# Kernel tuning notes

Measured on AMD Instinct MI355X. Metric: run time of the kernel, lower is better.

Reference implementation:

```python
import jax, jax.numpy as jnp
import numpy as np

B, N, D, H = 2, 2048, 384, 8
Dh = D // H          # 48
G = Dh // 3          # 16 3-vectors per head
EPS = 1e-5


def setup_inputs() -> dict:
    key = jax.random.key(0)
    ks = jax.random.split(key, 8)
    x = jax.random.normal(ks[0], (B, N, D), dtype=jnp.float32)
    # per-node SE(3) frames: proper rotation matrices via QR of random Gaussians
    raw = jax.random.normal(ks[1], (B, N, 3, 3), dtype=jnp.float32)
    q, r = jnp.linalg.qr(raw)
    sign = jnp.sign(jnp.diagonal(r, axis1=-2, axis2=-1))
    frames = q * sign[..., None, :]
    s = 1.0 / np.sqrt(D)
    Wq = jax.random.normal(ks[2], (D, D), dtype=jnp.float32) * s
    Wk = jax.random.normal(ks[3], (D, D), dtype=jnp.float32) * s
    Wv = jax.random.normal(ks[4], (D, D), dtype=jnp.float32) * s
    Wo = jax.random.normal(ks[5], (D, D), dtype=jnp.float32) * s
    bo = jnp.zeros((D,), dtype=jnp.float32)
    gamma = jnp.ones((D,), dtype=jnp.float32)
    beta = jnp.zeros((D,), dtype=jnp.float32)
    return {"x": x, "frames": frames, "Wq": Wq, "Wk": Wk, "Wv": Wv,
            "Wo": Wo, "bo": bo, "gamma": gamma, "beta": beta}


def _rotate(frames, t):
    # t: [B,N,H,Dh] -> rotate each 3-vector chunk by the node's frame R_i
    b, n, h, dh = t.shape
    t3 = t.reshape(b, n, h, dh // 3, 3)
    r3 = jnp.einsum('bnij,bnhgj->bnhgi', frames, t3)
    return r3.reshape(b, n, h, dh)


def reference(x, frames, Wq, Wk, Wv, Wo, bo, gamma, beta):
    b, n, d = x.shape
    Q = (x @ Wq.T).reshape(b, n, H, Dh)
    K = (x @ Wk.T).reshape(b, n, H, Dh)
    V = (x @ Wv.T).reshape(b, n, H, Dh)
    # SE(3) frame-conditioned attention: rotate Q,K into each node's local frame
    Qr = _rotate(frames, Q)
    Kr = _rotate(frames, K)
    scores = jnp.einsum('bqhd,bkhd->bhqk', Qr, Kr) / np.sqrt(Dh)
    attn = jax.nn.softmax(scores, axis=-1)
    out = jnp.einsum('bhqk,bkhd->bqhd', attn, V).reshape(b, n, d)
    out = out @ Wo.T + bo          # out_proj; dropout is identity in eval
    y = x + out                     # residual
    mu = jnp.mean(y, axis=-1, keepdims=True)
    var = jnp.var(y, axis=-1, keepdims=True)
    return (y - mu) * jax.lax.rsqrt(var + EPS) * gamma + beta
```

## Files before the change

kernel.cpp:

```cpp
#include <hip/hip_runtime.h>
#include <hip/hip_bf16.h>
#include <math.h>

constexpr int B = 2, N = 2048, D = 384, H = 8, Dh = 48;
constexpr int M = B * N;
constexpr float EPS = 1e-5f;
constexpr int WSZ = 384 * 384;

typedef short bf16x8 __attribute__((ext_vector_type(8)));
typedef float f32x4 __attribute__((ext_vector_type(4)));

#if __has_builtin(__builtin_amdgcn_exp2f)
#define EXP2(x) __builtin_amdgcn_exp2f(x)
#else
#define EXP2(x) exp2f(x)
#endif

__device__ __forceinline__ ushort f2bf(float f) {
  union { float f; uint u; } v; v.f = f;
  uint r = v.u + 0x7fffu + ((v.u >> 16) & 1u);
  return (ushort)(r >> 16);
}
__device__ __forceinline__ float bf2f(ushort u) {
  union { uint u; float f; } v; v.u = ((uint)u) << 16;
  return v.f;
}
__device__ __forceinline__ uint pk_bf16(float lo, float hi) {
  union { __hip_bfloat162 h; uint u; } v;
  v.h = __float22bfloat162_rn(make_float2(lo, hi));
  return v.u;
}

__device__ __forceinline__ void gload16(const void* g, void* lds) {
  __builtin_amdgcn_global_load_lds(
      (const __attribute__((address_space(1))) unsigned int*)g,
      (__attribute__((address_space(3))) unsigned int*)lds, 16, 0, 0);
}

__global__ __launch_bounds__(256) void pack_all(
    const float* __restrict__ x, const float* __restrict__ Wq,
    const float* __restrict__ Wk, const float* __restrict__ Wv,
    const float* __restrict__ Wo, ushort* __restrict__ xbf,
    ushort* __restrict__ Wqkv, ushort* __restrict__ Wobf) {
  constexpr int XSZ = M * 384;
  int i = (blockIdx.x * 256 + threadIdx.x) * 8;
  const float* src; ushort* dst; int off;
  if (i < XSZ) { src = x; dst = xbf; off = i; }
  else {
    int j = i - XSZ;
    if (j < WSZ)          { src = Wq; dst = Wqkv;           off = j; }
    else if (j < 2 * WSZ) { src = Wk; dst = Wqkv + WSZ;     off = j - WSZ; }
    else if (j < 3 * WSZ) { src = Wv; dst = Wqkv + 2 * WSZ; off = j - 2 * WSZ; }
    else                  { src = Wo; dst = Wobf;           off = j - 3 * WSZ; }
  }
  float4 a = *(const float4*)(src + off);
  float4 b = *(const float4*)(src + off + 4);
  uint4 o;
  o.x = pk_bf16(a.x, a.y);
  o.y = pk_bf16(a.z, a.w);
  o.z = pk_bf16(b.x, b.y);
  o.w = pk_bf16(b.z, b.w);
  *(uint4*)(dst + off) = o;
}

__global__ __launch_bounds__(256) void gemm_qkv(
    const ushort* __restrict__ Abf, const ushort* __restrict__ Wbf,
    const float* __restrict__ F, ushort* __restrict__ Qpad,
    ushort* __restrict__ Kpad, ushort* __restrict__ Vt, float qscale) {
  __shared__ __align__(16) ushort SH[128 * 96];
  ushort* Asm = SH;
  ushort* Bsm = SH + 4096;
  const int tid = threadIdx.x, w = tid >> 6, lane = tid & 63;
  const int lq = lane & 15, g = lane >> 4;
  const int brow = blockIdx.y * 128;
  const int bx = blockIdx.x;
  const int bcol = bx * 96;
  const int wr0 = (w >> 1) * 64, wc0 = (w & 1) * 48;
  const int srow = lane >> 2, scol = (lane & 3) * 8;

  f32x4 acc[4][3];
#pragma unroll
  for (int mi = 0; mi < 4; ++mi)
#pragma unroll
    for (int ni = 0; ni < 3; ++ni) acc[mi][ni] = f32x4{0.f, 0.f, 0.f, 0.f};

  for (int kt = 0; kt < 384; kt += 32) {
    __syncthreads();
    for (int s = w; s < 14; s += 4) {
      if (s < 8)
        gload16(Abf + (size_t)(brow + s * 16 + srow) * 384 + kt + scol, Asm + s * 512);
      else
        gload16(Wbf + (size_t)(bcol + (s - 8) * 16 + srow) * 384 + kt + scol,
                Bsm + (s - 8) * 512);
    }
    __syncthreads();
    bf16x8 a[4], b[3];
#pragma unroll
    for (int mi = 0; mi < 4; ++mi)
      a[mi] = *(const bf16x8*)(Asm + (wr0 + mi * 16 + lq) * 32 + g * 8);
#pragma unroll
    for (int ni = 0; ni < 3; ++ni)
      b[ni] = *(const bf16x8*)(Bsm + (wc0 + ni * 16 + lq) * 32 + g * 8);
#pragma unroll
    for (int mi = 0; mi < 4; ++mi)
#pragma unroll
      for (int ni = 0; ni < 3; ++ni)
        acc[mi][ni] = __builtin_amdgcn_mfma_f32_16x16x32_bf16(a[mi], b[ni], acc[mi][ni], 0, 0, 0);
  }

  if (bx >= 8) {
#pragma unroll
    for (int mi = 0; mi < 4; ++mi)
#pragma unroll
      for (int ni = 0; ni < 3; ++ni) {
        int vcol = (bx - 8) * 96 + wc0 + ni * 16 + lq;
        int hh = vcol / 48, dh = vcol - hh * 48;
#pragma unroll
        for (int r = 0; r < 4; ++r) {
          int row = brow + wr0 + mi * 16 + g * 4 + r;
          int bb = row >> 11, nn = row & 2047;
          Vt[((size_t)(bb * H + hh) * 48 + dh) * N + nn] = f2bf(acc[mi][ni][r]);
        }
      }
    return;
  }

  __syncthreads();
#pragma unroll
  for (int mi = 0; mi < 4; ++mi)
#pragma unroll
    for (int ni = 0; ni < 3; ++ni) {
      int col = wc0 + ni * 16 + lq;
#pragma unroll
      for (int r = 0; r < 4; ++r)
        SH[(wr0 + mi * 16 + g * 4 + r) * 96 + col] = f2bf(acc[mi][ni][r]);
    }
  __syncthreads();

  ushort* dstm = (bx < 4) ? Qpad : Kpad;
  const int hb = (bx & 3) * 2;
  const float scale = (bx < 4) ? qscale : 1.0f;
#pragma unroll
  for (int it = 0; it < 2; ++it) {
    int task = tid + it * 256;
    int row = task >> 2;
    int hh = (task >> 1) & 1;
    int half = task & 1;
    int bn = brow + row;
    const float* R = F + (size_t)bn * 9;
    float r0 = R[0], r1 = R[1], r2 = R[2];
    float r3 = R[3], r4 = R[4], r5 = R[5];
    float r6 = R[6], r7 = R[7], r8 = R[8];
    const ushort* src = SH + row * 96 + hh * 48 + half * 24;
    uint u[12];
    *(uint4*)(u)     = *(const uint4*)(src);
    *(uint4*)(u + 4) = *(const uint4*)(src + 8);
    *(uint4*)(u + 8) = *(const uint4*)(src + 16);
    float f[24];
#pragma unroll
    for (int j = 0; j < 12; ++j) {
      f[2 * j] = bf2f((ushort)u[j]);
      f[2 * j + 1] = bf2f((ushort)(u[j] >> 16));
    }
    float o[24];
#pragma unroll
    for (int t = 0; t < 8; ++t) {
      float v0 = f[3 * t], v1 = f[3 * t + 1], v2 = f[3 * t + 2];
      o[3 * t]     = (r0 * v0 + r1 * v1 + r2 * v2) * scale;
      o[3 * t + 1] = (r3 * v0 + r4 * v1 + r5 * v2) * scale;
      o[3 * t + 2] = (r6 * v0 + r7 * v1 + r8 * v2) * scale;
    }
    uint ow[12];
#pragma unroll
    for (int j = 0; j < 12; ++j) ow[j] = pk_bf16(o[2 * j], o[2 * j + 1]);
    ushort* dp = dstm + (size_t)bn * 512 + (hb + hh) * 64 + half * 24;
    *(uint4*)(dp)      = *(uint4*)(ow);
    *(uint4*)(dp + 8)  = *(uint4*)(ow + 4);
    *(uint4*)(dp + 16) = *(uint4*)(ow + 8);
    if (half) {
      uint4 z = make_uint4(0, 0, 0, 0);
      ushort* zp = dstm + (size_t)bn * 512 + (hb + hh) * 64 + 48;
      *(uint4*)(zp) = z;
      *(uint4*)(zp + 8) = z;
    }
  }
}

__global__ __launch_bounds__(128) void attn_mfma(
    const ushort* __restrict__ Qpad, const ushort* __restrict__ Kpad,
    const ushort* __restrict__ Vt, ushort* __restrict__ Pacc,
    float* __restrict__ Pml) {
  __shared__ __align__(16) ushort SH[8192];
  ushort* K0 = SH;
  ushort* K1 = SH + 4096;

  const int bid = blockIdx.x;
  const int wg = (bid & 7) * 128 + (bid >> 3);
  const int qt = wg & 31;
  const int rest = wg >> 5;
  const int h = rest & 7;
  const int b = (rest >> 3) & 1;
  const int half = rest >> 4;
  const int kt0 = half * 1024;
  const int tid = threadIdx.x;
  const int w = tid >> 6;
  const int lane = tid & 63;
  const int lq = lane & 15;
  const int g = lane >> 4;
  const int l7 = lq & 7;
  const int srow8 = lane >> 3;
  const int c8 = (lane & 7) ^ srow8;

  bf16x8 qf[2][2];
  {
    const ushort* qb = Qpad + ((size_t)(b * N) + qt * 64 + w * 32) * 512 + h * 64;
#pragma unroll
    for (int i = 0; i < 2; ++i)
#pragma unroll
      for (int kd = 0; kd < 2; ++kd)
        qf[i][kd] = *(const bf16x8*)(qb + (size_t)(i * 16 + lq) * 512 + kd * 32 + g * 8);
  }

  const ushort* kg[4];
#pragma unroll
  for (int j = 0; j < 4; ++j) {
    int s = w + 2 * j;
    int ki = (s >> 2) * 32 + (s & 1) * 16 + (srow8 >> 2) * 8 + ((s >> 1) & 1) * 4 + (srow8 & 3);
    kg[j] = Kpad + ((size_t)(b * N) + kt0 + ki) * 512 + h * 64 + c8 * 8;
  }
  const ushort* vbase = Vt + ((size_t)(b * H + h) * 48 + lq) * (size_t)N + kt0 + g * 8;

  auto stage = [&](ushort* kb) {
#pragma unroll
    for (int j = 0; j < 4; ++j) {
      gload16(kg[j], kb + (w + 2 * j) * 512);
      kg[j] += 64 * 512;
    }
  };

  float m[2] = {-3.0e38f, -3.0e38f}, l[2] = {0.f, 0.f};
  f32x4 oacc[2][3];
#pragma unroll
  for (int i = 0; i < 2; ++i)
#pragma unroll
    for (int d = 0; d < 3; ++d) oacc[i][d] = f32x4{0.f, 0.f, 0.f, 0.f};

  stage(K0);
  __syncthreads();
  int cur = 0;

  for (int t = 0; t < 16; ++t) {
    if (t < 15) stage(cur ? K0 : K1);
    const ushort* Kc = cur ? K1 : K0;

    bf16x8 vf[2][3];
#pragma unroll
    for (int ks = 0; ks < 2; ++ks)
#pragma unroll
      for (int d = 0; d < 3; ++d)
        vf[ks][d] = *(const bf16x8*)(vbase + (size_t)(d * 16) * N + ks * 32);

    f32x4 st[2][4];
#pragma unroll
    for (int i = 0; i < 2; ++i)
#pragma unroll
      for (int t4 = 0; t4 < 4; ++t4) st[i][t4] = f32x4{0.f, 0.f, 0.f, 0.f};
#pragma unroll
    for (int t4 = 0; t4 < 4; ++t4) {
      bf16x8 a0 = *(const bf16x8*)(Kc + (t4 * 16 + lq) * 64 + ((g ^ l7) * 8));
      bf16x8 a1 = *(const bf16x8*)(Kc + (t4 * 16 + lq) * 64 + (((g + 4) ^ l7) * 8));
#pragma unroll
      for (int i = 0; i < 2; ++i) {
        st[i][t4] = __builtin_amdgcn_mfma_f32_16x16x32_bf16(a0, qf[i][0], st[i][t4], 0, 0, 0);
        st[i][t4] = __builtin_amdgcn_mfma_f32_16x16x32_bf16(a1, qf[i][1], st[i][t4], 0, 0, 0);
      }
    }

    float tmax[2];
#pragma unroll
    for (int i = 0; i < 2; ++i) {
      float t0 = st[i][0][0];
#pragma unroll
      for (int t4 = 0; t4 < 4; ++t4)
#pragma unroll
        for (int r = 0; r < 4; ++r) t0 = fmaxf(t0, st[i][t4][r]);
      t0 = fmaxf(t0, __shfl_xor(t0, 16));
      t0 = fmaxf(t0, __shfl_xor(t0, 32));
      tmax[i] = t0;
    }
    bool need = (tmax[0] > m[0] + 8.0f) | (tmax[1] > m[1] + 8.0f);
    if (__ballot(need)) {
#pragma unroll
      for (int i = 0; i < 2; ++i) {
        float mnew = fmaxf(m[i], tmax[i]);
        float corr = EXP2(m[i] - mnew);
        m[i] = mnew;
        l[i] *= corr;
#pragma unroll
        for (int r = 0; r < 4; ++r) {
          float cr = __shfl(corr, g * 4 + r);
#pragma unroll
          for (int d = 0; d < 3; ++d) oacc[i][d][r] *= cr;
        }
      }
    }

    bf16x8 pf[2][2];
#pragma unroll
    for (int i = 0; i < 2; ++i) {
      float ps = 0.f;
      uint u0[4], u1[4];
#pragma unroll
      for (int t4 = 0; t4 < 4; ++t4) {
        float p0 = EXP2(st[i][t4][0] - m[i]);
        float p1 = EXP2(st[i][t4][1] - m[i]);
        float p2 = EXP2(st[i][t4][2] - m[i]);
        float p3 = EXP2(st[i][t4][3] - m[i]);
        ps += (p0 + p1) + (p2 + p3);
        if (t4 < 2) {
          u0[(t4 & 1) * 2]     = pk_bf16(p0, p1);
          u0[(t4 & 1) * 2 + 1] = pk_bf16(p2, p3);
        } else {
          u1[(t4 & 1) * 2]     = pk_bf16(p0, p1);
          u1[(t4 & 1) * 2 + 1] = pk_bf16(p2, p3);
        }
      }
      ps += __shfl_xor(ps, 16);
      ps += __shfl_xor(ps, 32);
      l[i] += ps;
      union { uint4 q; bf16x8 v; } c0, c1;
      c0.q = make_uint4(u0[0], u0[1], u0[2], u0[3]);
      c1.q = make_uint4(u1[0], u1[1], u1[2], u1[3]);
      pf[i][0] = c0.v;
      pf[i][1] = c1.v;
    }

#pragma unroll
    for (int ks = 0; ks < 2; ++ks)
#pragma unroll
      for (int i = 0; i < 2; ++i)
#pragma unroll
        for (int d = 0; d < 3; ++d)
          oacc[i][d] = __builtin_amdgcn_mfma_f32_16x16x32_bf16(pf[i][ks], vf[ks][d], oacc[i][d], 0, 0, 0);

    vbase += 64;
    __syncthreads();
    cur ^= 1;
  }

#pragma unroll
  for (int i = 0; i < 2; ++i) {
    const size_t pr0 = ((size_t)((half * B + b) * H + h)) * N + qt * 64 + (w * 2 + i) * 16;
#pragma unroll
    for (int d = 0; d < 3; ++d)
#pragma unroll
      for (int r = 0; r < 4; ++r)
        Pacc[(pr0 + g * 4 + r) * 48 + d * 16 + lq] = f2bf(oacc[i][d][r]);
    if (g == 0) {
      Pml[(pr0 + lq) * 2] = m[i];
      Pml[(pr0 + lq) * 2 + 1] = l[i];
    }
  }
}

__global__ __launch_bounds__(256) void gemm_out_ln(
    const ushort* __restrict__ Pacc, const float* __restrict__ Pml,
    const ushort* __restrict__ Wbf, const float* __restrict__ x,
    const float* __restrict__ bo, const float* __restrict__ gamma,
    const float* __restrict__ beta, float* __restrict__ out) {
  __shared__ ushort Asm[16 * 32];
  __shared__ ushort Bsm[384 * 32];
  __shared__ float red[4][16][2];
  __shared__ float Wm[16][8][2];
  const int tid = threadIdx.x, w = tid >> 6, lane = tid & 63;
  const int lq = lane & 15, g = lane >> 4;
  const int brow = blockIdx.x * 16;
  const int srow = lane >> 2, scol = (lane & 3) * 8;

  if (tid < 128) {
    int r = tid >> 3, hh = tid & 7;
    int gr = brow + r;
    int bb = gr >> 11, nn = gr & 2047;
    size_t i0 = ((size_t)(bb * H + hh)) * N + nn;
    size_t i1 = ((size_t)((B + bb) * H + hh)) * N + nn;
    float m0 = Pml[i0 * 2], l0 = Pml[i0 * 2 + 1];
    float m1 = Pml[i1 * 2], l1 = Pml[i1 * 2 + 1];
    float mm = fmaxf(m0, m1);
    float e0 = EXP2(m0 - mm), e1 = EXP2(m1 - mm);
    float inv = 1.f / (l0 * e0 + l1 * e1);
    Wm[r][hh][0] = e0 * inv;
    Wm[r][hh][1] = e1 * inv;
  }
  __syncthreads();

  f32x4 acc[6];
#pragma unroll
  for (int ni = 0; ni < 6; ++ni) acc[ni] = f32x4{0.f, 0.f, 0.f, 0.f};

  for (int kt = 0; kt < 384; kt += 32) {
    __syncthreads();
    if (w == 0) {
      int col = kt + scol;
      int hh = col / 48;
      int dcol = col - hh * 48;
      int gr = brow + srow;
      int bb = gr >> 11, nn = gr & 2047;
      const ushort* a0p = Pacc + (((size_t)(bb * H + hh)) * N + nn) * 48 + dcol;
      const ushort* a1p = Pacc + (((size_t)((B + bb) * H + hh)) * N + nn) * 48 + dcol;
      bf16x8 a0 = *(const bf16x8*)a0p;
      bf16x8 a1 = *(const bf16x8*)a1p;
      float w0v = Wm[srow][hh][0], w1v = Wm[srow][hh][1];
      uint mg[4];
#pragma unroll
      for (int j = 0; j < 4; ++j)
        mg[j] = pk_bf16(
            bf2f((ushort)a0[2 * j]) * w0v + bf2f((ushort)a1[2 * j]) * w1v,
            bf2f((ushort)a0[2 * j + 1]) * w0v + bf2f((ushort)a1[2 * j + 1]) * w1v);
      *(uint4*)(Asm + srow * 32 + scol) = make_uint4(mg[0], mg[1], mg[2], mg[3]);
    }
#pragma unroll
    for (int i = 0; i < 6; ++i) {
      int seg = w * 6 + i;
      gload16(Wbf + (size_t)(seg * 16 + srow) * 384 + kt + scol, Bsm + seg * 512);
    }
    __syncthreads();
    bf16x8 a = *(const bf16x8*)(Asm + lq * 32 + g * 8);
#pragma unroll
    for (int ni = 0; ni < 6; ++ni) {
      bf16x8 bb2 = *(const bf16x8*)(Bsm + ((w * 6 + ni) * 16 + lq) * 32 + g * 8);
      acc[ni] = __builtin_amdgcn_mfma_f32_16x16x32_bf16(a, bb2, acc[ni], 0, 0, 0);
    }
  }

  float s[4] = {0.f, 0.f, 0.f, 0.f}, s2[4] = {0.f, 0.f, 0.f, 0.f};
#pragma unroll
  for (int ni = 0; ni < 6; ++ni) {
    int col = (w * 6 + ni) * 16 + lq;
    float bcol = bo[col];
#pragma unroll
    for (int r = 0; r < 4; ++r) {
      float y = acc[ni][r] + x[(size_t)(brow + g * 4 + r) * 384 + col] + bcol;
      acc[ni][r] = y;
      s[r] += y; s2[r] += y * y;
    }
  }
#pragma unroll
  for (int o = 1; o < 16; o <<= 1) {
#pragma unroll
    for (int r = 0; r < 4; ++r) {
      s[r] += __shfl_xor(s[r], o);
      s2[r] += __shfl_xor(s2[r], o);
    }
  }
  if (lq == 0) {
#pragma unroll
    for (int r = 0; r < 4; ++r) {
      red[w][g * 4 + r][0] = s[r];
      red[w][g * 4 + r][1] = s2[r];
    }
  }
  __syncthreads();
#pragma unroll
  for (int r = 0; r < 4; ++r) {
    int row = g * 4 + r;
    float ts  = red[0][row][0] + red[1][row][0] + red[2][row][0] + red[3][row][0];
    float ts2 = red[0][row][1] + red[1][row][1] + red[2][row][1] + red[3][row][1];
    float mu = ts * (1.f / 384.f);
    float var = ts2 * (1.f / 384.f) - mu * mu;
    float rstd = rsqrtf(var + EPS);
    float* orow = out + (size_t)(brow + row) * 384;
#pragma unroll
    for (int ni = 0; ni < 6; ++ni) {
      int col = (w * 6 + ni) * 16 + lq;
      orow[col] = (acc[ni][r] - mu) * rstd * gamma[col] + beta[col];
    }
  }
}

extern "C" void kernel_launch(void* const* d_in, const int* in_sizes, int n_in,
                              void* d_out, int out_size, void* d_ws, size_t ws_size,
                              hipStream_t stream) {
  const float* x      = (const float*)d_in[0];
  const float* frames = (const float*)d_in[1];
  const float* Wq     = (const float*)d_in[2];
  const float* Wk     = (const float*)d_in[3];
  const float* Wv     = (const float*)d_in[4];
  const float* Wo     = (const float*)d_in[5];
  const float* bo     = (const float*)d_in[6];
  const float* gamma  = (const float*)d_in[7];
  const float* beta   = (const float*)d_in[8];
  float* out = (float*)d_out;

  ushort* xbf  = (ushort*)d_ws;
  ushort* Wqkv = xbf + (size_t)M * 384;
  ushort* Wobf = Wqkv + 3 * (size_t)WSZ;
  ushort* Qpad = Wobf + (size_t)WSZ;
  ushort* Kpad = Qpad + (size_t)M * 512;
  ushort* Vt   = Kpad + (size_t)M * 512;
  ushort* Pacc = Vt + (size_t)M * 384;
  float*  Pml  = (float*)(Pacc + (size_t)2 * B * H * N * 48);

  const float qscale = 0.14433756729740643f * 1.4426950408889634f;

  pack_all<<<(M * 384 + 4 * WSZ) / (8 * 256), 256, 0, stream>>>(
      x, Wq, Wk, Wv, Wo, xbf, Wqkv, Wobf);

  gemm_qkv<<<dim3(12, 32), 256, 0, stream>>>(xbf, Wqkv, frames, Qpad, Kpad, Vt, qscale);

  attn_mfma<<<2 * B * H * (N / 64), 128, 0, stream>>>(Qpad, Kpad, Vt, Pacc, Pml);

  gemm_out_ln<<<M / 16, 256, 0, stream>>>(Pacc, Pml, Wobf, x, bo, gamma, beta, out);
}
```

Measured before the change: 74.31 us.

## Fuse fp32-to-bf16 packing into GEMM loads and drop the pack kernel

Removes the separate pack_all kernel. gemm_qkv and gemm_out_ln now load fp32 x and weight tiles straight into XOR-swizzled LDS and convert them to bf16 while reading MFMA fragments. gemm_qkv's row tile is halved to 64 and the grid doubled, which keeps more blocks in flight. This saves one launch and the round trip through bf16 staging buffers, at the cost of twice the global and LDS traffic per tile and repeated per-block conversion of Wo and the QKV weights.

```diff
diff --git a/kernel.cpp b/kernel.cpp
--- a/kernel.cpp
+++ b/kernel.cpp
@@ -5,7 +5,6 @@
 constexpr int B = 2, N = 2048, D = 384, H = 8, Dh = 48;
 constexpr int M = B * N;
 constexpr float EPS = 1e-5f;
-constexpr int WSZ = 384 * 384;
 
 typedef short bf16x8 __attribute__((ext_vector_type(8)));
 typedef float f32x4 __attribute__((ext_vector_type(4)));
@@ -37,72 +36,66 @@
       (__attribute__((address_space(3))) unsigned int*)lds, 16, 0, 0);
 }
 
-__global__ __launch_bounds__(256) void pack_all(
-    const float* __restrict__ x, const float* __restrict__ Wq,
+__device__ __forceinline__ bf16x8 readFragF(const float* base, int row, int g) {
+  int rx = row & 7;
+  const f32x4 lo = *(const f32x4*)(base + row * 32 + (((2 * g) ^ rx) * 4));
+  const f32x4 hi = *(const f32x4*)(base + row * 32 + (((2 * g + 1) ^ rx) * 4));
+  union { uint4 q; bf16x8 v; } c;
+  c.q.x = pk_bf16(lo[0], lo[1]);
+  c.q.y = pk_bf16(lo[2], lo[3]);
+  c.q.z = pk_bf16(hi[0], hi[1]);
+  c.q.w = pk_bf16(hi[2], hi[3]);
+  return c.v;
+}
+
+__global__ __launch_bounds__(256) void gemm_qkv(
+    const float* __restrict__ Xf, const float* __restrict__ Wq,
     const float* __restrict__ Wk, const float* __restrict__ Wv,
-    const float* __restrict__ Wo, ushort* __restrict__ xbf,
-    ushort* __restrict__ Wqkv, ushort* __restrict__ Wobf) {
-  constexpr int XSZ = M * 384;
-  int i = (blockIdx.x * 256 + threadIdx.x) * 8;
-  const float* src; ushort* dst; int off;
-  if (i < XSZ) { src = x; dst = xbf; off = i; }
-  else {
-    int j = i - XSZ;
-    if (j < WSZ)          { src = Wq; dst = Wqkv;           off = j; }
-    else if (j < 2 * WSZ) { src = Wk; dst = Wqkv + WSZ;     off = j - WSZ; }
-    else if (j < 3 * WSZ) { src = Wv; dst = Wqkv + 2 * WSZ; off = j - 2 * WSZ; }
-    else                  { src = Wo; dst = Wobf;           off = j - 3 * WSZ; }
-  }
-  float4 a = *(const float4*)(src + off);
-  float4 b = *(const float4*)(src + off + 4);
-  uint4 o;
-  o.x = pk_bf16(a.x, a.y);
-  o.y = pk_bf16(a.z, a.w);
-  o.z = pk_bf16(b.x, b.y);
-  o.w = pk_bf16(b.z, b.w);
-  *(uint4*)(dst + off) = o;
-}
-
-__global__ __launch_bounds__(256) void gemm_qkv(
-    const ushort* __restrict__ Abf, const ushort* __restrict__ Wbf,
     const float* __restrict__ F, ushort* __restrict__ Qpad,
     ushort* __restrict__ Kpad, ushort* __restrict__ Vt, float qscale) {
-  __shared__ __align__(16) ushort SH[128 * 96];
-  ushort* Asm = SH;
-  ushort* Bsm = SH + 4096;
+  __shared__ __align__(16) float SHf[5120];
+  float* Af = SHf;
+  float* Bf = SHf + 2048;
+  ushort* Cb = (ushort*)SHf;
+
   const int tid = threadIdx.x, w = tid >> 6, lane = tid & 63;
   const int lq = lane & 15, g = lane >> 4;
-  const int brow = blockIdx.y * 128;
+  const int brow = blockIdx.y * 64;
   const int bx = blockIdx.x;
-  const int bcol = bx * 96;
-  const int wr0 = (w >> 1) * 64, wc0 = (w & 1) * 48;
-  const int srow = lane >> 2, scol = (lane & 3) * 8;
-
-  f32x4 acc[4][3];
-#pragma unroll
-  for (int mi = 0; mi < 4; ++mi)
+  const float* Wsrc = (bx < 4) ? Wq : ((bx < 8) ? Wk : Wv);
+  const int wrow = (bx & 3) * 96;
+  const int wr0 = (w >> 1) * 32, wc0 = (w & 1) * 48;
+  const int r8 = lane >> 3;
+  const int cs = ((lane & 7) ^ r8) * 4;
+
+  f32x4 acc[2][3];
+#pragma unroll
+  for (int mi = 0; mi < 2; ++mi)
 #pragma unroll
     for (int ni = 0; ni < 3; ++ni) acc[mi][ni] = f32x4{0.f, 0.f, 0.f, 0.f};
 
   for (int kt = 0; kt < 384; kt += 32) {
     __syncthreads();
-    for (int s = w; s < 14; s += 4) {
-      if (s < 8)
-        gload16(Abf + (size_t)(brow + s * 16 + srow) * 384 + kt + scol, Asm + s * 512);
-      else
-        gload16(Wbf + (size_t)(bcol + (s - 8) * 16 + srow) * 384 + kt + scol,
-                Bsm + (s - 8) * 512);
+#pragma unroll
+    for (int j = 0; j < 2; ++j) {
+      int u = w + 4 * j;
+      gload16(Xf + (size_t)(brow + u * 8 + r8) * 384 + kt + cs, Af + u * 256);
+    }
+#pragma unroll
+    for (int j = 0; j < 3; ++j) {
+      int u = w + 4 * j;
+      gload16(Wsrc + (size_t)(wrow + u * 8 + r8) * 384 + kt + cs, Bf + u * 256);
     }
     __syncthreads();
-    bf16x8 a[4], b[3];
-#pragma unroll
-    for (int mi = 0; mi < 4; ++mi)
-      a[mi] = *(const bf16x8*)(Asm + (wr0 + mi * 16 + lq) * 32 + g * 8);
+    bf16x8 a[2], b[3];
+#pragma unroll
+    for (int mi = 0; mi < 2; ++mi)
+      a[mi] = readFragF(Af, wr0 + mi * 16 + lq, g);
 #pragma unroll
     for (int ni = 0; ni < 3; ++ni)
-      b[ni] = *(const bf16x8*)(Bsm + (wc0 + ni * 16 + lq) * 32 + g * 8);
-#pragma unroll
-    for (int mi = 0; mi < 4; ++mi)
+      b[ni] = readFragF(Bf, wc0 + ni * 16 + lq, g);
+#pragma unroll
+    for (int mi = 0; mi < 2; ++mi)
 #pragma unroll
       for (int ni = 0; ni < 3; ++ni)
         acc[mi][ni] = __builtin_amdgcn_mfma_f32_16x16x32_bf16(a[mi], b[ni], acc[mi][ni], 0, 0, 0);
@@ -110,7 +103,7 @@
 
   if (bx >= 8) {
 #pragma unroll
-    for (int mi = 0; mi < 4; ++mi)
+    for (int mi = 0; mi < 2; ++mi)
 #pragma unroll
       for (int ni = 0; ni < 3; ++ni) {
         int vcol = (bx - 8) * 96 + wc0 + ni * 16 + lq;
@@ -127,22 +120,21 @@
 
   __syncthreads();
 #pragma unroll
-  for (int mi = 0; mi < 4; ++mi)
+  for (int mi = 0; mi < 2; ++mi)
 #pragma unroll
     for (int ni = 0; ni < 3; ++ni) {
       int col = wc0 + ni * 16 + lq;
 #pragma unroll
       for (int r = 0; r < 4; ++r)
-        SH[(wr0 + mi * 16 + g * 4 + r) * 96 + col] = f2bf(acc[mi][ni][r]);
+        Cb[(wr0 + mi * 16 + g * 4 + r) * 96 + col] = f2bf(acc[mi][ni][r]);
     }
   __syncthreads();
 
   ushort* dstm = (bx < 4) ? Qpad : Kpad;
   const int hb = (bx & 3) * 2;
   const float scale = (bx < 4) ? qscale : 1.0f;
-#pragma unroll
-  for (int it = 0; it < 2; ++it) {
-    int task = tid + it * 256;
+  {
+    int task = tid;
     int row = task >> 2;
     int hh = (task >> 1) & 1;
     int half = task & 1;
@@ -150,8 +142,8 @@
     const float* R = F + (size_t)bn * 9;
     float r0 = R[0], r1 = R[1], r2 = R[2];
     float r3 = R[3], r4 = R[4], r5 = R[5];
-    float r6 = R[6], r7 = R[7], r8 = R[8];
-    const ushort* src = SH + row * 96 + hh * 48 + half * 24;
+    float r6 = R[6], r7 = R[7], r8f = R[8];
+    const ushort* src = Cb + row * 96 + hh * 48 + half * 24;
     uint u[12];
     *(uint4*)(u)     = *(const uint4*)(src);
     *(uint4*)(u + 4) = *(const uint4*)(src + 8);
@@ -168,7 +160,7 @@
       float v0 = f[3 * t], v1 = f[3 * t + 1], v2 = f[3 * t + 2];
       o[3 * t]     = (r0 * v0 + r1 * v1 + r2 * v2) * scale;
       o[3 * t + 1] = (r3 * v0 + r4 * v1 + r5 * v2) * scale;
-      o[3 * t + 2] = (r6 * v0 + r7 * v1 + r8 * v2) * scale;
+      o[3 * t + 2] = (r6 * v0 + r7 * v1 + r8f * v2) * scale;
     }
     uint ow[12];
 #pragma unroll
@@ -365,17 +357,19 @@
 
 __global__ __launch_bounds__(256) void gemm_out_ln(
     const ushort* __restrict__ Pacc, const float* __restrict__ Pml,
-    const ushort* __restrict__ Wbf, const float* __restrict__ x,
+    const float* __restrict__ Wo, const float* __restrict__ x,
     const float* __restrict__ bo, const float* __restrict__ gamma,
     const float* __restrict__ beta, float* __restrict__ out) {
+  __shared__ __align__(16) float Bf[12288];
   __shared__ ushort Asm[16 * 32];
-  __shared__ ushort Bsm[384 * 32];
   __shared__ float red[4][16][2];
   __shared__ float Wm[16][8][2];
   const int tid = threadIdx.x, w = tid >> 6, lane = tid & 63;
   const int lq = lane & 15, g = lane >> 4;
   const int brow = blockIdx.x * 16;
   const int srow = lane >> 2, scol = (lane & 3) * 8;
+  const int r8 = lane >> 3;
+  const int cs = ((lane & 7) ^ r8) * 4;
 
   if (tid < 128) {
     int r = tid >> 3, hh = tid & 7;
@@ -419,15 +413,15 @@
       *(uint4*)(Asm + srow * 32 + scol) = make_uint4(mg[0], mg[1], mg[2], mg[3]);
     }
 #pragma unroll
-    for (int i = 0; i < 6; ++i) {
-      int seg = w * 6 + i;
-      gload16(Wbf + (size_t)(seg * 16 + srow) * 384 + kt + scol, Bsm + seg * 512);
+    for (int j = 0; j < 12; ++j) {
+      int u = w + 4 * j;
+      gload16(Wo + (size_t)(u * 8 + r8) * 384 + kt + cs, Bf + u * 256);
     }
     __syncthreads();
     bf16x8 a = *(const bf16x8*)(Asm + lq * 32 + g * 8);
 #pragma unroll
     for (int ni = 0; ni < 6; ++ni) {
-      bf16x8 bb2 = *(const bf16x8*)(Bsm + ((w * 6 + ni) * 16 + lq) * 32 + g * 8);
+      bf16x8 bb2 = readFragF(Bf, (w * 6 + ni) * 16 + lq, g);
       acc[ni] = __builtin_amdgcn_mfma_f32_16x16x32_bf16(a, bb2, acc[ni], 0, 0, 0);
     }
   }
@@ -491,10 +485,7 @@
   const float* beta   = (const float*)d_in[8];
   float* out = (float*)d_out;
 
-  ushort* xbf  = (ushort*)d_ws;
-  ushort* Wqkv = xbf + (size_t)M * 384;
-  ushort* Wobf = Wqkv + 3 * (size_t)WSZ;
-  ushort* Qpad = Wobf + (size_t)WSZ;
+  ushort* Qpad = (ushort*)d_ws;
   ushort* Kpad = Qpad + (size_t)M * 512;
   ushort* Vt   = Kpad + (size_t)M * 512;
   ushort* Pacc = Vt + (size_t)M * 384;
@@ -502,12 +493,10 @@
 
   const float qscale = 0.14433756729740643f * 1.4426950408889634f;
 
-  pack_all<<<(M * 384 + 4 * WSZ) / (8 * 256), 256, 0, stream>>>(
-      x, Wq, Wk, Wv, Wo, xbf, Wqkv, Wobf);
-
-  gemm_qkv<<<dim3(12, 32), 256, 0, stream>>>(xbf, Wqkv, frames, Qpad, Kpad, Vt, qscale);
+  gemm_qkv<<<dim3(12, 64), 256, 0, stream>>>(
+      x, Wq, Wk, Wv, frames, Qpad, Kpad, Vt, qscale);
 
   attn_mfma<<<2 * B * H * (N / 64), 128, 0, stream>>>(Qpad, Kpad, Vt, Pacc, Pml);
 
-  gemm_out_ln<<<M / 16, 256, 0, stream>>>(Pacc, Pml, Wobf, x, bo, gamma, beta, out);
-}
+  gemm_out_ln<<<M / 16, 256, 0, stream>>>(Pacc, Pml, Wo, x, bo, gamma, beta, out);
+}
```

Result: faster. 72.64 us (-2.3%).
